# Kernel optimization log

Measured on AMD Instinct MI355X. Metric: run time of the kernel, lower is better.

Reference implementation:

```python
import jax, jax.numpy as jnp
import numpy as np

# static architecture constants
NUM_GRAPHS = 64
NODES_PER_GRAPH = 512
N_TOTAL = NUM_GRAPHS * NODES_PER_GRAPH          # 32768
AVG_DEG = 16
E_TOTAL = N_TOTAL * AVG_DEG                      # 524288
NODE_NUMBER = 1000
EMB = 128
DIMF = 128
NUM_LAYERS = 4
K = 64
DIM_TARGET = 2
LATENT = NUM_LAYERS * DIMF + 1                   # 513


def setup_inputs() -> dict:
    key = jax.random.key(0)
    ks = jax.random.split(key, 16)
    # node ids
    x = jax.random.randint(ks[0], (N_TOTAL,), 0, NODE_NUMBER, dtype=jnp.int32)
    # edges confined within each graph
    epg = NODES_PER_GRAPH * AVG_DEG
    src_l = jax.random.randint(ks[1], (NUM_GRAPHS, epg), 0, NODES_PER_GRAPH, dtype=jnp.int32)
    dst_l = jax.random.randint(ks[2], (NUM_GRAPHS, epg), 0, NODES_PER_GRAPH, dtype=jnp.int32)
    off = (jnp.arange(NUM_GRAPHS, dtype=jnp.int32) * NODES_PER_GRAPH)[:, None]
    edge_index = jnp.stack([(src_l + off).reshape(-1), (dst_l + off).reshape(-1)])  # [2,E]
    batch = jnp.repeat(jnp.arange(NUM_GRAPHS, dtype=jnp.int32), NODES_PER_GRAPH)

    def lin(k, fi, fo):
        return jax.random.normal(k, (fi, fo), jnp.float32) / np.sqrt(fi)

    emb = jax.random.normal(ks[3], (NODE_NUMBER, EMB), jnp.float32)
    W_convs = jnp.stack([lin(jax.random.fold_in(ks[4], l), EMB if l == 0 else DIMF, DIMF)
                         for l in range(NUM_LAYERS)])            # [L,128,128]
    b_convs = jnp.zeros((NUM_LAYERS, DIMF), jnp.float32)
    W_last = lin(ks[5], DIMF, 1)
    b_last = jnp.zeros((1,), jnp.float32)
    conv1_w = jax.random.normal(ks[6], (16, 1, LATENT), jnp.float32) / np.sqrt(LATENT)
    conv1_b = jnp.zeros((16,), jnp.float32)
    conv2_w = jax.random.normal(ks[7], (32, 16, 5), jnp.float32) / np.sqrt(16 * 5)
    conv2_b = jnp.zeros((32,), jnp.float32)
    dd = (K - 2) // 2 + 1                      # 32
    in_dense = (dd - 5 + 1) * 32               # 896
    d1_w = lin(ks[8], in_dense, dd)
    d1_b = jnp.zeros((dd,), jnp.float32)
    d2_w = lin(ks[9], dd, DIM_TARGET)
    d2_b = jnp.zeros((DIM_TARGET,), jnp.float32)
    return dict(x=x, edge_index=edge_index, batch=batch, emb=emb,
                W_convs=W_convs, b_convs=b_convs, W_last=W_last, b_last=b_last,
                conv1_w=conv1_w, conv1_b=conv1_b, conv2_w=conv2_w, conv2_b=conv2_b,
                d1_w=d1_w, d1_b=d1_b, d2_w=d2_w, d2_b=d2_b)


def _gcn(h, W, b, src, dst, norm):
    # linear -> gather -> degree-normalize -> scatter-add (DGCNNConv with aggr='add')
    h = h @ W + b
    msg = h[src] * norm[:, None]
    return jax.ops.segment_sum(msg, dst, num_segments=N_TOTAL)


def reference(x, edge_index, batch, emb, W_convs, b_convs, W_last, b_last,
              conv1_w, conv1_b, conv2_w, conv2_b, d1_w, d1_b, d2_w, d2_b):
    loops = jnp.arange(N_TOTAL, dtype=edge_index.dtype)
    src = jnp.concatenate([edge_index[0], loops])
    dst = jnp.concatenate([edge_index[1], loops])
    # deg = degree(src); norm = deg^-1 gathered at dst (as in DGCNNConv.message)
    deg = jax.ops.segment_sum(jnp.ones_like(src, jnp.float32), src, num_segments=N_TOTAL)
    norm = (1.0 / deg)[dst]

    h = emb[x]                                           # [N,128]
    hidden = []
    for l in range(NUM_LAYERS):
        h = jnp.tanh(_gcn(h, W_convs[l], b_convs[l], src, dst, norm))
        hidden.append(h)
    h = jnp.tanh(_gcn(h, W_last, b_last, src, dst, norm))  # [N,1]
    hidden.append(h)
    xcat = jnp.concatenate(hidden, axis=1)               # [N, 513]

    # global_sort_pool: batch is sorted with equal-size graphs -> dense reshape
    x3 = xcat.reshape(NUM_GRAPHS, NODES_PER_GRAPH, LATENT)
    order = jnp.argsort(-x3[..., -1], axis=1)[:, :K]     # descending by last channel, top-k
    pooled = jnp.take_along_axis(x3, order[:, :, None], axis=1)  # [B,K,513]

    # conv1d(1,16,kernel=513,stride=513) over [B,1,K*513] == per-row projection
    y1 = jax.nn.relu(jnp.einsum('bkd,od->bok', pooled, conv1_w[:, 0, :])
                     + conv1_b[None, :, None])           # [B,16,K]
    L = K // 2
    y1 = y1.reshape(NUM_GRAPHS, 16, L, 2).max(axis=-1)   # maxpool(2,2)
    y2 = jax.lax.conv_general_dilated(y1, conv2_w, (1,), 'VALID',
                                      dimension_numbers=('NCH', 'OIH', 'NCH'))
    y2 = jax.nn.relu(y2 + conv2_b[None, :, None])        # [B,32,L-4]
    flat = y2.reshape(NUM_GRAPHS, -1)                    # [B,896]
    h1 = jax.nn.relu(flat @ d1_w + d1_b)                 # dropout is identity in eval
    logits = h1 @ d2_w + d2_b
    return jax.nn.softmax(logits, axis=-1)
```

## Files before the change

### kernel.cpp

```cpp
#include <hip/hip_runtime.h>
#include <hip/hip_bf16.h>
#include <math.h>

#define N_TOTAL 32768
#define E_TOTAL 524288
#define NUM_GRAPHS 64
#define NPG 512
#define EMB 128
#define MAXD 64
#define KTOP 64
#define LATENT 513
#define PPAD 524


__global__ __launch_bounds__(256) void k_init(int* __restrict__ deg, int* __restrict__ cnt) {
    int i = blockIdx.x * 256 + threadIdx.x;
    if (i < N_TOTAL) { deg[i] = 1; cnt[i] = 0; }
}

__global__ __launch_bounds__(256) void k_build(const int* __restrict__ ei,
                                               int* __restrict__ deg, int* __restrict__ cnt,
                                               int* __restrict__ adj) {
    int e = blockIdx.x * 256 + threadIdx.x;
    if (e >= E_TOTAL) return;
    int s = ei[e];
    int d = ei[E_TOTAL + e];
    atomicAdd(&deg[s], 1);
    int slot = atomicAdd(&cnt[d], 1);
    if (slot < MAXD) adj[(size_t)d * MAXD + slot] = s;
}


__global__ __launch_bounds__(256) void k_agg0(const int* __restrict__ x,
                                              const float* __restrict__ emb,
                                              float* __restrict__ Agg,
                                              const int* __restrict__ adj,
                                              const int* __restrict__ cnt) {
    int bid = blockIdx.x;
    int xcd = bid & 7;
    int j = bid >> 3;
    int g = (xcd << 3) + (j >> 7);
    int chunk = j & 127;
    int wv = threadIdx.x >> 6, lane = threadIdx.x & 63;
    int v = g * NPG + chunk * 4 + wv;

    int c = cnt[v]; if (c > MAXD) c = MAXD;
    const int* av = adj + (size_t)v * MAXD;
    int nb = (lane < c) ? av[lane] : v;
    int xnb = x[nb];
    const float2* e2 = (const float2*)emb;
    float2 s = e2[(size_t)x[v] * 64 + lane];
    for (int i = 0; i < c; ++i) {
        int u = __shfl(xnb, i);
        float2 t = e2[(size_t)u * 64 + lane];
        s.x += t.x; s.y += t.y;
    }
    ((float2*)Agg)[(size_t)v * 64 + lane] = s;
}

__global__ __launch_bounds__(256) void k_agg(const float* __restrict__ Hin,
                                             float* __restrict__ Agg,
                                             const int* __restrict__ adj,
                                             const int* __restrict__ cnt) {
    int bid = blockIdx.x;
    int xcd = bid & 7;
    int j = bid >> 3;
    int g = (xcd << 3) + (j >> 7);
    int chunk = j & 127;
    int wv = threadIdx.x >> 6, lane = threadIdx.x & 63;
    int v = g * NPG + chunk * 4 + wv;

    int c = cnt[v]; if (c > MAXD) c = MAXD;
    const int* av = adj + (size_t)v * MAXD;
    int nb = (lane < c) ? av[lane] : 0;
    const float2* hin = (const float2*)Hin;
    float2 s = hin[(size_t)v * 64 + lane];
    for (int i = 0; i < c; ++i) {
        int u = __shfl(nb, i);
        float2 t = hin[(size_t)u * 64 + lane];
        s.x += t.x; s.y += t.y;
    }
    ((float2*)Agg)[(size_t)v * 64 + lane] = s;
}


__global__ __launch_bounds__(256) void k_gemm_tanh(const float* __restrict__ Agg,
                                                   const float* __restrict__ W,
                                                   const float* __restrict__ bvec,
                                                   float* __restrict__ Hout,
                                                   const int* __restrict__ cnt,
                                                   const int* __restrict__ deg) {
    __shared__ float As[128][68];
    __shared__ float Ws[64][64];
    int tid = threadIdx.x;
    int bid = blockIdx.x;
    int rb = bid >> 1, cbk = bid & 1;
    int tc = tid & 7;
    int tr = tid >> 3;
    float acc[4][8];
#pragma unroll
    for (int i = 0; i < 4; ++i)
#pragma unroll
        for (int jj = 0; jj < 8; ++jj) acc[i][jj] = 0.f;

    for (int st = 0; st < 2; ++st) {
#pragma unroll
        for (int it = 0; it < 8; ++it) {
            int idx = tid + it * 256;
            int r = idx >> 4, c4 = idx & 15;
            float4 a = *(const float4*)(Agg + (size_t)(rb * 128 + r) * 128 + st * 64 + c4 * 4);
            *(float4*)&As[r][c4 * 4] = a;
        }
#pragma unroll
        for (int it = 0; it < 4; ++it) {
            int idx = tid + it * 256;
            int kk = idx >> 4, c4 = idx & 15;
            float4 w = *(const float4*)(W + (size_t)(st * 64 + kk) * 128 + cbk * 64 + c4 * 4);
            *(float4*)&Ws[kk][c4 * 4] = w;
        }
        __syncthreads();

        int tr4 = tr * 4, tc8 = tc * 8;
#pragma unroll
        for (int kk = 0; kk < 64; kk += 4) {
            float a[4][4];
            *(float4*)&a[0][0] = *(const float4*)&As[tr4 + 0][kk];
            *(float4*)&a[1][0] = *(const float4*)&As[tr4 + 1][kk];
            *(float4*)&a[2][0] = *(const float4*)&As[tr4 + 2][kk];
            *(float4*)&a[3][0] = *(const float4*)&As[tr4 + 3][kk];
            float w[4][8];
#pragma unroll
            for (int q = 0; q < 4; ++q) {
                *(float4*)&w[q][0] = *(const float4*)&Ws[kk + q][tc8];
                *(float4*)&w[q][4] = *(const float4*)&Ws[kk + q][tc8 + 4];
            }
#pragma unroll
            for (int q = 0; q < 4; ++q)
#pragma unroll
                for (int i = 0; i < 4; ++i)
#pragma unroll
                    for (int jj = 0; jj < 8; ++jj)
                        acc[i][jj] = fmaf(a[i][q], w[q][jj], acc[i][jj]);
        }
        __syncthreads();
    }

    int r0 = rb * 128 + tr * 4;
    int c0 = cbk * 64 + tc * 8;
#pragma unroll
    for (int i = 0; i < 4; ++i) {
        int r = r0 + i;
        float invd = 1.0f / (float)deg[r];
        float cp1 = (float)(cnt[r] + 1);
        float o[8];
#pragma unroll
        for (int jj = 0; jj < 8; ++jj)
            o[jj] = tanhf((acc[i][jj] + bvec[c0 + jj] * cp1) * invd);
        *(float4*)(Hout + (size_t)r * 128 + c0)     = make_float4(o[0], o[1], o[2], o[3]);
        *(float4*)(Hout + (size_t)r * 128 + c0 + 4) = make_float4(o[4], o[5], o[6], o[7]);
    }
}


__global__ __launch_bounds__(256) void k_last_lin(const float* __restrict__ H4,
                                                  const float* __restrict__ Wl,
                                                  const float* __restrict__ bl,
                                                  float* __restrict__ tmp) {
    int wv = threadIdx.x >> 6, lane = threadIdx.x & 63;
    int v = blockIdx.x * 4 + wv;
    float2 h = ((const float2*)H4)[(size_t)v * 64 + lane];
    float2 w = ((const float2*)Wl)[lane];
    float s = h.x * w.x + h.y * w.y;
#pragma unroll
    for (int off = 32; off > 0; off >>= 1) s += __shfl_xor(s, off);
    if (lane == 0) tmp[v] = s + bl[0];
}

__global__ __launch_bounds__(256) void k_last_agg(const float* __restrict__ tmp,
                                                  const int* __restrict__ adj,
                                                  const int* __restrict__ cnt,
                                                  const int* __restrict__ deg,
                                                  float* __restrict__ lastc) {
    int v = blockIdx.x * 256 + threadIdx.x;
    if (v >= N_TOTAL) return;
    float s = tmp[v];
    int c = cnt[v]; if (c > MAXD) c = MAXD;
    const int* av = adj + (size_t)v * MAXD;
    for (int i = 0; i < c; ++i) s += tmp[av[i]];
    lastc[v] = tanhf(s / (float)deg[v]);
}


__global__ __launch_bounds__(256) void k_sort(const float* __restrict__ lastc,
                                              int* __restrict__ topk) {
    __shared__ float v[512];
    __shared__ int ix[512];
    int g = blockIdx.x, tid = threadIdx.x;
    for (int i = tid; i < 512; i += 256) { v[i] = lastc[g * NPG + i]; ix[i] = i; }
    __syncthreads();
    for (int ksz = 2; ksz <= 512; ksz <<= 1) {
        for (int jj = ksz >> 1; jj > 0; jj >>= 1) {
            for (int i = tid; i < 512; i += 256) {
                int p = i ^ jj;
                if (p > i) {
                    float va = v[i], vb = v[p];
                    int ia = ix[i], ib = ix[p];
                    bool b_before_a = (vb > va) || (vb == va && ib < ia);
                    bool up = (i & ksz) == 0;
                    bool sw = up ? b_before_a : !b_before_a;
                    if (sw) { v[i] = vb; v[p] = va; ix[i] = ib; ix[p] = ia; }
                }
            }
            __syncthreads();
        }
    }
    for (int k = tid; k < KTOP; k += 256) topk[g * KTOP + k] = g * NPG + ix[k];
}


__global__ __launch_bounds__(256) void k_conv1(const int* __restrict__ topk,
                                               const float* __restrict__ h0,
                                               const float* __restrict__ h1,
                                               const float* __restrict__ h2,
                                               const float* __restrict__ h3,
                                               const float* __restrict__ lastc,
                                               const float* __restrict__ c1w,
                                               const float* __restrict__ c1b,
                                               float* __restrict__ y1p) {
    __shared__ float P[16][PPAD];
    __shared__ float Y1c[16][16];
    __shared__ int nodes[16];
    int bid = blockIdx.x;
    int g = bid >> 2, cc = bid & 3;
    int tid = threadIdx.x;
    if (tid < 16) nodes[tid] = topk[g * KTOP + cc * 16 + tid];
    __syncthreads();

    {
        int r = tid >> 4, t4 = tid & 15;
        int node = nodes[r];
#pragma unroll
        for (int jj = 0; jj < 8; ++jj) {
            int d = (t4 + 16 * jj) * 4;
            const float* src = (d < 128) ? h0 : (d < 256) ? h1 : (d < 384) ? h2 : h3;
            float4 val = *(const float4*)(src + (size_t)node * 128 + (d & 127));
            *(float4*)&P[r][d] = val;
        }
        if (t4 == 0) P[r][512] = lastc[node];
    }
    __syncthreads();

    int o = tid >> 4, kk = tid & 15;
    const float* w = c1w + (size_t)o * LATENT;
    float a0 = 0.f, a1 = 0.f, a2 = 0.f, a3 = 0.f;
    for (int d = 0; d < 512; d += 4) {
        float4 p = *(const float4*)&P[kk][d];
        a0 = fmaf(p.x, w[d],     a0);
        a1 = fmaf(p.y, w[d + 1], a1);
        a2 = fmaf(p.z, w[d + 2], a2);
        a3 = fmaf(p.w, w[d + 3], a3);
    }
    float s = ((a0 + a1) + (a2 + a3)) + P[kk][512] * w[512] + c1b[o];
    Y1c[o][kk] = fmaxf(s, 0.f);
    __syncthreads();

    if (tid < 128) {
        int oo = tid >> 3, l = tid & 7;
        y1p[(size_t)g * 512 + oo * 32 + cc * 8 + l] = fmaxf(Y1c[oo][2 * l], Y1c[oo][2 * l + 1]);
    }
}


__global__ __launch_bounds__(256) void k_tail(const float* __restrict__ y1p,
                                              const float* __restrict__ c2w, const float* __restrict__ c2b,
                                              const float* __restrict__ d1w, const float* __restrict__ d1b,
                                              const float* __restrict__ d2w, const float* __restrict__ d2b,
                                              float* __restrict__ out) {
    __shared__ float Y1P[16][32];
    __shared__ float Y2[32][28];
    __shared__ float H1s[32];
    __shared__ float red[256];
    int g = blockIdx.x, tid = threadIdx.x;

    for (int t = tid; t < 512; t += 256) ((float*)Y1P)[t] = y1p[(size_t)g * 512 + t];
    __syncthreads();

    for (int t = tid; t < 32 * 28; t += 256) {
        int o2 = t / 28, tt = t - o2 * 28;
        float s = c2b[o2];
#pragma unroll
        for (int i = 0; i < 16; ++i)
#pragma unroll
            for (int dt = 0; dt < 5; ++dt)
                s = fmaf(Y1P[i][tt + dt], c2w[o2 * 80 + i * 5 + dt], s);
        Y2[o2][tt] = fmaxf(s, 0.f);
    }
    __syncthreads();

    {
        int jcol = tid >> 3, part = tid & 7;
        float s = 0.f;
        for (int rr = 0; rr < 4; ++rr) {
            int o2 = part * 4 + rr;
            int base = o2 * 28;
            for (int tt = 0; tt < 28; ++tt)
                s = fmaf(Y2[o2][tt], d1w[(size_t)(base + tt) * 32 + jcol], s);
        }
        red[tid] = s;
        __syncthreads();
        if (part == 0) {
            float t = 0.f;
#pragma unroll
            for (int p = 0; p < 8; ++p) t += red[tid + p];
            H1s[jcol] = fmaxf(t + d1b[jcol], 0.f);
        }
        __syncthreads();
    }

    if (tid == 0) {
        float l0 = d2b[0], l1 = d2b[1];
        for (int jc = 0; jc < 32; ++jc) {
            l0 = fmaf(H1s[jc], d2w[jc * 2 + 0], l0);
            l1 = fmaf(H1s[jc], d2w[jc * 2 + 1], l1);
        }
        float m = fmaxf(l0, l1);
        float e0 = expf(l0 - m), e1 = expf(l1 - m);
        float inv = 1.f / (e0 + e1);
        out[g * 2 + 0] = e0 * inv;
        out[g * 2 + 1] = e1 * inv;
    }
}


extern "C" void kernel_launch(void* const* d_in, const int* in_sizes, int n_in,
                              void* d_out, int out_size, void* d_ws, size_t ws_size,
                              hipStream_t stream) {
    const int*   x    = (const int*)d_in[0];
    const int*   ei   = (const int*)d_in[1];
    const float* emb  = (const float*)d_in[3];
    const float* Wc   = (const float*)d_in[4];
    const float* bc   = (const float*)d_in[5];
    const float* Wl   = (const float*)d_in[6];
    const float* bl   = (const float*)d_in[7];
    const float* c1w  = (const float*)d_in[8];
    const float* c1b  = (const float*)d_in[9];
    const float* c2w  = (const float*)d_in[10];
    const float* c2b  = (const float*)d_in[11];
    const float* d1w  = (const float*)d_in[12];
    const float* d1b  = (const float*)d_in[13];
    const float* d2w  = (const float*)d_in[14];
    const float* d2b  = (const float*)d_in[15];
    float* out = (float*)d_out;

    char* ws = (char*)d_ws;
    int*   deg  = (int*)ws;            ws += (size_t)N_TOTAL * 4;
    int*   cnt  = (int*)ws;            ws += (size_t)N_TOTAL * 4;
    int*   adj  = (int*)ws;            ws += (size_t)N_TOTAL * MAXD * 4;
    float* Agg  = (float*)ws;          ws += (size_t)N_TOTAL * 128 * 4;
    float* Hid0 = (float*)ws;          ws += (size_t)N_TOTAL * 128 * 4;
    float* Hid1 = (float*)ws;          ws += (size_t)N_TOTAL * 128 * 4;
    float* Hid2 = (float*)ws;          ws += (size_t)N_TOTAL * 128 * 4;
    float* Hid3 = (float*)ws;          ws += (size_t)N_TOTAL * 128 * 4;
    float* tmp  = (float*)ws;          ws += (size_t)N_TOTAL * 4;
    float* lastc= (float*)ws;          ws += (size_t)N_TOTAL * 4;
    int*   topk = (int*)ws;            ws += (size_t)NUM_GRAPHS * KTOP * 4;
    float* y1p  = (float*)ws;          ws += (size_t)NUM_GRAPHS * 16 * 32 * 4;

    k_init <<<N_TOTAL / 256, 256, 0, stream>>>(deg, cnt);
    k_build<<<E_TOTAL / 256, 256, 0, stream>>>(ei, deg, cnt, adj);

    float* Hids[4] = {Hid0, Hid1, Hid2, Hid3};
    for (int l = 0; l < 4; ++l) {
        if (l == 0)
            k_agg0<<<N_TOTAL / 4, 256, 0, stream>>>(x, emb, Agg, adj, cnt);
        else
            k_agg<<<N_TOTAL / 4, 256, 0, stream>>>(Hids[l - 1], Agg, adj, cnt);
        k_gemm_tanh<<<(N_TOTAL / 128) * 2, 256, 0, stream>>>(Agg, Wc + (size_t)l * 128 * 128,
                                                             bc + (size_t)l * 128, Hids[l], cnt, deg);
    }
    k_last_lin<<<N_TOTAL / 4, 256, 0, stream>>>(Hid3, Wl, bl, tmp);
    k_last_agg<<<N_TOTAL / 256, 256, 0, stream>>>(tmp, adj, cnt, deg, lastc);
    k_sort<<<NUM_GRAPHS, 256, 0, stream>>>(lastc, topk);
    k_conv1<<<NUM_GRAPHS * 4, 256, 0, stream>>>(topk, Hid0, Hid1, Hid2, Hid3, lastc, c1w, c1b, y1p);
    k_tail<<<NUM_GRAPHS, 256, 0, stream>>>(y1p, c2w, c2b, d1w, d1b, d2w, d2b, out);
}
```

Before: 359.2 us.

## Fuse neighbor aggregation with split-bf16 MFMA GEMM and tanh per layer

Replaces the separate aggregation and FP32 SIMT GEMM kernels with one per-layer kernel. It gathers neighbor sums into shared memory as hi/lo bf16 pairs and multiplies with a pre-transposed split-bf16 weight using three MFMA 16x16x32 ops, which approximates FP32 accuracy. The final layer also folds in the last linear projection. This drops the Agg round trip through global memory and the extra launches, and moves the matmul onto matrix cores. The cost is 512 blocks with serial per-wave gathers, which lowers parallelism in the memory-bound aggregation phase.

```diff
diff --git a/kernel.cpp b/kernel.cpp
--- a/kernel.cpp
+++ b/kernel.cpp
@@ -11,6 +11,17 @@
 #define KTOP 64
 #define LATENT 513
 #define PPAD 524
+
+typedef __attribute__((ext_vector_type(8))) short bf16x8;
+typedef __attribute__((ext_vector_type(4))) float f32x4;
+
+__device__ __forceinline__ unsigned short f2bf(float f) {
+    unsigned u = __float_as_uint(f);
+    return (unsigned short)((u + 0x7FFFu + ((u >> 16) & 1u)) >> 16);
+}
+__device__ __forceinline__ float bf2f(unsigned short h) {
+    return __uint_as_float(((unsigned)h) << 16);
+}
 
 
 __global__ __launch_bounds__(256) void k_init(int* __restrict__ deg, int* __restrict__ cnt) {
@@ -31,150 +42,146 @@
 }
 
 
-__global__ __launch_bounds__(256) void k_agg0(const int* __restrict__ x,
-                                              const float* __restrict__ emb,
-                                              float* __restrict__ Agg,
-                                              const int* __restrict__ adj,
-                                              const int* __restrict__ cnt) {
+__global__ __launch_bounds__(256) void k_prep(const float* __restrict__ Wc,
+                                              unsigned short* __restrict__ Wth,
+                                              unsigned short* __restrict__ Wtl) {
+    __shared__ float tile[64][65];
+    int b = blockIdx.x;
+    int l = b >> 2, t = b & 3;
+    int k0 = (t >> 1) * 64, o0 = (t & 1) * 64;
+    int lane = threadIdx.x & 63, q = threadIdx.x >> 6;
+    const float* Wsrc = Wc + (size_t)l * 16384;
+#pragma unroll
+    for (int it = 0; it < 16; ++it) {
+        int r = it * 4 + q;
+        tile[r][lane] = Wsrc[(size_t)(k0 + r) * 128 + o0 + lane];
+    }
+    __syncthreads();
+#pragma unroll
+    for (int it = 0; it < 16; ++it) {
+        int o = it * 4 + q;
+        float v = tile[lane][o];
+        unsigned short h = f2bf(v);
+        unsigned short lo = f2bf(v - bf2f(h));
+        size_t dst = (size_t)l * 16384 + (size_t)(o0 + o) * 128 + k0 + lane;
+        Wth[dst] = h; Wtl[dst] = lo;
+    }
+}
+
+
+__global__ __launch_bounds__(256) void k_layer(const int* __restrict__ xids,
+                                               const float* __restrict__ Hin,
+                                               const unsigned short* __restrict__ Wth,
+                                               const unsigned short* __restrict__ Wtl,
+                                               const float* __restrict__ bvec,
+                                               const float* __restrict__ Wl,
+                                               const float* __restrict__ bl,
+                                               float* __restrict__ tmp,
+                                               float* __restrict__ Hout,
+                                               const int* __restrict__ adj,
+                                               const int* __restrict__ cnt,
+                                               const int* __restrict__ deg) {
+    __shared__ unsigned char smem[32768];
+    int tid = threadIdx.x;
+    int w = tid >> 6, lane = tid & 63;
     int bid = blockIdx.x;
-    int xcd = bid & 7;
-    int j = bid >> 3;
-    int g = (xcd << 3) + (j >> 7);
-    int chunk = j & 127;
-    int wv = threadIdx.x >> 6, lane = threadIdx.x & 63;
-    int v = g * NPG + chunk * 4 + wv;
-
-    int c = cnt[v]; if (c > MAXD) c = MAXD;
-    const int* av = adj + (size_t)v * MAXD;
-    int nb = (lane < c) ? av[lane] : v;
-    int xnb = x[nb];
-    const float2* e2 = (const float2*)emb;
-    float2 s = e2[(size_t)x[v] * 64 + lane];
-    for (int i = 0; i < c; ++i) {
-        int u = __shfl(xnb, i);
-        float2 t = e2[(size_t)u * 64 + lane];
-        s.x += t.x; s.y += t.y;
-    }
-    ((float2*)Agg)[(size_t)v * 64 + lane] = s;
-}
-
-__global__ __launch_bounds__(256) void k_agg(const float* __restrict__ Hin,
-                                             float* __restrict__ Agg,
-                                             const int* __restrict__ adj,
-                                             const int* __restrict__ cnt) {
-    int bid = blockIdx.x;
-    int xcd = bid & 7;
-    int j = bid >> 3;
-    int g = (xcd << 3) + (j >> 7);
-    int chunk = j & 127;
-    int wv = threadIdx.x >> 6, lane = threadIdx.x & 63;
-    int v = g * NPG + chunk * 4 + wv;
-
-    int c = cnt[v]; if (c > MAXD) c = MAXD;
-    const int* av = adj + (size_t)v * MAXD;
-    int nb = (lane < c) ? av[lane] : 0;
-    const float2* hin = (const float2*)Hin;
-    float2 s = hin[(size_t)v * 64 + lane];
-    for (int i = 0; i < c; ++i) {
-        int u = __shfl(nb, i);
-        float2 t = hin[(size_t)u * 64 + lane];
-        s.x += t.x; s.y += t.y;
-    }
-    ((float2*)Agg)[(size_t)v * 64 + lane] = s;
-}
-
-
-__global__ __launch_bounds__(256) void k_gemm_tanh(const float* __restrict__ Agg,
-                                                   const float* __restrict__ W,
-                                                   const float* __restrict__ bvec,
-                                                   float* __restrict__ Hout,
-                                                   const int* __restrict__ cnt,
-                                                   const int* __restrict__ deg) {
-    __shared__ float As[128][68];
-    __shared__ float Ws[64][64];
-    int tid = threadIdx.x;
-    int bid = blockIdx.x;
-    int rb = bid >> 1, cbk = bid & 1;
-    int tc = tid & 7;
-    int tr = tid >> 3;
-    float acc[4][8];
-#pragma unroll
-    for (int i = 0; i < 4; ++i)
-#pragma unroll
-        for (int jj = 0; jj < 8; ++jj) acc[i][jj] = 0.f;
-
-    for (int st = 0; st < 2; ++st) {
-#pragma unroll
-        for (int it = 0; it < 8; ++it) {
-            int idx = tid + it * 256;
-            int r = idx >> 4, c4 = idx & 15;
-            float4 a = *(const float4*)(Agg + (size_t)(rb * 128 + r) * 128 + st * 64 + c4 * 4);
-            *(float4*)&As[r][c4 * 4] = a;
-        }
-#pragma unroll
-        for (int it = 0; it < 4; ++it) {
-            int idx = tid + it * 256;
-            int kk = idx >> 4, c4 = idx & 15;
-            float4 w = *(const float4*)(W + (size_t)(st * 64 + kk) * 128 + cbk * 64 + c4 * 4);
-            *(float4*)&Ws[kk][c4 * 4] = w;
-        }
-        __syncthreads();
-
-        int tr4 = tr * 4, tc8 = tc * 8;
-#pragma unroll
-        for (int kk = 0; kk < 64; kk += 4) {
-            float a[4][4];
-            *(float4*)&a[0][0] = *(const float4*)&As[tr4 + 0][kk];
-            *(float4*)&a[1][0] = *(const float4*)&As[tr4 + 1][kk];
-            *(float4*)&a[2][0] = *(const float4*)&As[tr4 + 2][kk];
-            *(float4*)&a[3][0] = *(const float4*)&As[tr4 + 3][kk];
-            float w[4][8];
-#pragma unroll
-            for (int q = 0; q < 4; ++q) {
-                *(float4*)&w[q][0] = *(const float4*)&Ws[kk + q][tc8];
-                *(float4*)&w[q][4] = *(const float4*)&Ws[kk + q][tc8 + 4];
+    int xcd = bid & 7, j = bid >> 3;
+    int g = (xcd << 3) + (j >> 3);
+    int chunk = j & 7;
+    int rowbase = g * NPG + chunk * 64 + w * 16;
+    const float2* h2 = (const float2*)Hin;
+
+    for (int i = 0; i < 16; i += 2) {
+        int va = rowbase + i, vb = va + 1;
+        int ca = cnt[va]; if (ca > MAXD) ca = MAXD;
+        int cb = cnt[vb]; if (cb > MAXD) cb = MAXD;
+        const int* Aa = adj + (size_t)va * MAXD;
+        const int* Ab = adj + (size_t)vb * MAXD;
+        int na = (lane < ca) ? Aa[lane] : 0;
+        int nb = (lane < cb) ? Ab[lane] : 0;
+        int ia = va, ib = vb;
+        if (xids) {
+            na = (lane < ca) ? xids[na] : 0;
+            nb = (lane < cb) ? xids[nb] : 0;
+            ia = xids[va]; ib = xids[vb];
+        }
+        float2 sa = h2[(size_t)ia * 64 + lane];
+        float2 sb = h2[(size_t)ib * 64 + lane];
+        int mx = ca > cb ? ca : cb;
+        for (int t = 0; t < mx; ++t) {
+            if (t < ca) { float2 v = h2[(size_t)__shfl(na, t) * 64 + lane]; sa.x += v.x; sa.y += v.y; }
+            if (t < cb) { float2 v = h2[(size_t)__shfl(nb, t) * 64 + lane]; sb.x += v.x; sb.y += v.y; }
+        }
+#pragma unroll
+        for (int p = 0; p < 2; ++p) {
+            float2 s = p ? sb : sa;
+            int r = w * 16 + i + p;
+            unsigned short hx = f2bf(s.x), hy = f2bf(s.y);
+            unsigned short lx = f2bf(s.x - bf2f(hx)), ly = f2bf(s.y - bf2f(hy));
+            int byte = r * 256 + ((lane * 4) ^ ((r & 7) << 4));
+            *(unsigned*)(smem + byte)         = (unsigned)hx | ((unsigned)hy << 16);
+            *(unsigned*)(smem + 16384 + byte) = (unsigned)lx | ((unsigned)ly << 16);
+        }
+    }
+    __syncthreads();
+
+    int r = lane & 15, kb = lane >> 4;
+    bf16x8 ah[4], al[4];
+#pragma unroll
+    for (int ks = 0; ks < 4; ++ks) {
+        int byte = (w * 16 + r) * 256 + (((ks * 64 + kb * 16)) ^ ((r & 7) << 4));
+        ah[ks] = *(const bf16x8*)(smem + byte);
+        al[ks] = *(const bf16x8*)(smem + 16384 + byte);
+    }
+    float invd[4], cp1[4];
+#pragma unroll
+    for (int q = 0; q < 4; ++q) {
+        int nd = rowbase + kb * 4 + q;
+        invd[q] = 1.0f / (float)deg[nd];
+        cp1[q]  = (float)(cnt[nd] + 1);
+    }
+    float ls0 = 0.f, ls1 = 0.f, ls2 = 0.f, ls3 = 0.f;
+    for (int ct = 0; ct < 8; ++ct) {
+        const unsigned short* Wh = Wth + (size_t)(ct * 16 + r) * 128;
+        const unsigned short* Wo = Wtl + (size_t)(ct * 16 + r) * 128;
+        f32x4 a = {0.f, 0.f, 0.f, 0.f};
+#pragma unroll
+        for (int ks = 0; ks < 4; ++ks) {
+            bf16x8 wh = *(const bf16x8*)(Wh + ks * 32 + kb * 8);
+            bf16x8 wl = *(const bf16x8*)(Wo + ks * 32 + kb * 8);
+            a = __builtin_amdgcn_mfma_f32_16x16x32_bf16(ah[ks], wh, a, 0, 0, 0);
+            a = __builtin_amdgcn_mfma_f32_16x16x32_bf16(ah[ks], wl, a, 0, 0, 0);
+            a = __builtin_amdgcn_mfma_f32_16x16x32_bf16(al[ks], wh, a, 0, 0, 0);
+        }
+        float bcol = bvec[ct * 16 + r];
+        float wlast = Wl ? Wl[ct * 16 + r] : 0.f;
+#pragma unroll
+        for (int q = 0; q < 4; ++q) {
+            float val = tanhf((a[q] + bcol * cp1[q]) * invd[q]);
+            Hout[(size_t)(rowbase + kb * 4 + q) * 128 + ct * 16 + r] = val;
+            if (Wl) {
+                float z = val * wlast;
+                if (q == 0) ls0 += z; else if (q == 1) ls1 += z;
+                else if (q == 2) ls2 += z; else ls3 += z;
             }
-#pragma unroll
-            for (int q = 0; q < 4; ++q)
-#pragma unroll
-                for (int i = 0; i < 4; ++i)
-#pragma unroll
-                    for (int jj = 0; jj < 8; ++jj)
-                        acc[i][jj] = fmaf(a[i][q], w[q][jj], acc[i][jj]);
-        }
-        __syncthreads();
-    }
-
-    int r0 = rb * 128 + tr * 4;
-    int c0 = cbk * 64 + tc * 8;
-#pragma unroll
-    for (int i = 0; i < 4; ++i) {
-        int r = r0 + i;
-        float invd = 1.0f / (float)deg[r];
-        float cp1 = (float)(cnt[r] + 1);
-        float o[8];
-#pragma unroll
-        for (int jj = 0; jj < 8; ++jj)
-            o[jj] = tanhf((acc[i][jj] + bvec[c0 + jj] * cp1) * invd);
-        *(float4*)(Hout + (size_t)r * 128 + c0)     = make_float4(o[0], o[1], o[2], o[3]);
-        *(float4*)(Hout + (size_t)r * 128 + c0 + 4) = make_float4(o[4], o[5], o[6], o[7]);
-    }
-}
-
-
-__global__ __launch_bounds__(256) void k_last_lin(const float* __restrict__ H4,
-                                                  const float* __restrict__ Wl,
-                                                  const float* __restrict__ bl,
-                                                  float* __restrict__ tmp) {
-    int wv = threadIdx.x >> 6, lane = threadIdx.x & 63;
-    int v = blockIdx.x * 4 + wv;
-    float2 h = ((const float2*)H4)[(size_t)v * 64 + lane];
-    float2 w = ((const float2*)Wl)[lane];
-    float s = h.x * w.x + h.y * w.y;
-#pragma unroll
-    for (int off = 32; off > 0; off >>= 1) s += __shfl_xor(s, off);
-    if (lane == 0) tmp[v] = s + bl[0];
-}
+        }
+    }
+    if (Wl) {
+#pragma unroll
+        for (int m = 1; m < 16; m <<= 1) {
+            ls0 += __shfl_xor(ls0, m); ls1 += __shfl_xor(ls1, m);
+            ls2 += __shfl_xor(ls2, m); ls3 += __shfl_xor(ls3, m);
+        }
+        if (r == 0) {
+            float b0 = bl[0];
+            tmp[rowbase + kb * 4 + 0] = ls0 + b0;
+            tmp[rowbase + kb * 4 + 1] = ls1 + b0;
+            tmp[rowbase + kb * 4 + 2] = ls2 + b0;
+            tmp[rowbase + kb * 4 + 3] = ls3 + b0;
+        }
+    }
+}
+
 
 __global__ __launch_bounds__(256) void k_last_agg(const float* __restrict__ tmp,
                                                   const int* __restrict__ adj,
@@ -356,11 +363,12 @@
     int*   deg  = (int*)ws;            ws += (size_t)N_TOTAL * 4;
     int*   cnt  = (int*)ws;            ws += (size_t)N_TOTAL * 4;
     int*   adj  = (int*)ws;            ws += (size_t)N_TOTAL * MAXD * 4;
-    float* Agg  = (float*)ws;          ws += (size_t)N_TOTAL * 128 * 4;
     float* Hid0 = (float*)ws;          ws += (size_t)N_TOTAL * 128 * 4;
     float* Hid1 = (float*)ws;          ws += (size_t)N_TOTAL * 128 * 4;
     float* Hid2 = (float*)ws;          ws += (size_t)N_TOTAL * 128 * 4;
     float* Hid3 = (float*)ws;          ws += (size_t)N_TOTAL * 128 * 4;
+    unsigned short* Wth = (unsigned short*)ws;  ws += (size_t)4 * 128 * 128 * 2;
+    unsigned short* Wtl = (unsigned short*)ws;  ws += (size_t)4 * 128 * 128 * 2;
     float* tmp  = (float*)ws;          ws += (size_t)N_TOTAL * 4;
     float* lastc= (float*)ws;          ws += (size_t)N_TOTAL * 4;
     int*   topk = (int*)ws;            ws += (size_t)NUM_GRAPHS * KTOP * 4;
@@ -368,17 +376,20 @@
 
     k_init <<<N_TOTAL / 256, 256, 0, stream>>>(deg, cnt);
     k_build<<<E_TOTAL / 256, 256, 0, stream>>>(ei, deg, cnt, adj);
+    k_prep <<<16, 256, 0, stream>>>(Wc, Wth, Wtl);
 
     float* Hids[4] = {Hid0, Hid1, Hid2, Hid3};
     for (int l = 0; l < 4; ++l) {
-        if (l == 0)
-            k_agg0<<<N_TOTAL / 4, 256, 0, stream>>>(x, emb, Agg, adj, cnt);
-        else
-            k_agg<<<N_TOTAL / 4, 256, 0, stream>>>(Hids[l - 1], Agg, adj, cnt);
-        k_gemm_tanh<<<(N_TOTAL / 128) * 2, 256, 0, stream>>>(Agg, Wc + (size_t)l * 128 * 128,
-                                                             bc + (size_t)l * 128, Hids[l], cnt, deg);
-    }
-    k_last_lin<<<N_TOTAL / 4, 256, 0, stream>>>(Hid3, Wl, bl, tmp);
+        const int*   xl  = (l == 0) ? x : nullptr;
+        const float* hin = (l == 0) ? emb : Hids[l - 1];
+        const float* wl  = (l == 3) ? Wl : nullptr;
+        const float* blp = (l == 3) ? bl : nullptr;
+        float*       tp  = (l == 3) ? tmp : nullptr;
+        k_layer<<<512, 256, 0, stream>>>(xl, hin,
+                                         Wth + (size_t)l * 16384, Wtl + (size_t)l * 16384,
+                                         bc + (size_t)l * 128, wl, blp, tp,
+                                         Hids[l], adj, cnt, deg);
+    }
     k_last_agg<<<N_TOTAL / 256, 256, 0, stream>>>(tmp, adj, cnt, deg, lastc);
     k_sort<<<NUM_GRAPHS, 256, 0, stream>>>(lastc, topk);
     k_conv1<<<NUM_GRAPHS * 4, 256, 0, stream>>>(topk, Hid0, Hid1, Hid2, Hid3, lastc, c1w, c1b, y1p);
```

New measurement: 479.8 us. 33.6% more time.
